# Optimization experiments

Hardware: AMD Instinct MI355X
Metric: run time of the kernel (lower is better)

## Reference

```python
import jax, jax.numpy as jnp
import numpy as np

GRID_SIZE = 25
DAMPING = 0.01


def setup_inputs() -> dict:
    key = jax.random.key(0)
    k1, k2 = jax.random.split(key)
    local_x = jax.random.normal(k1, (1, 4, 1000, 1000), dtype=jnp.float32)
    ms_history = jax.random.normal(k2, (1, 16, 4, 1000, 1000), dtype=jnp.float32)
    return {"local_x": local_x, "ms_history": ms_history}


def _project(local_x, ms_history):
    new_hist = ms_history[0]                      # (nt, nb, nx, ny)
    nt, nb, nx, ny = new_hist.shape
    nb2 = local_x.shape[1]
    ngs = GRID_SIZE
    ngx, ngy = nx // ngs, ny // ngs
    K, P = nb * nt, ngs * ngs
    # tile-ize: (ngx, ngy, K, P) and (ngx, ngy, nb2, P)
    V = new_hist.reshape(K, ngx, ngs, ngy, ngs).transpose(1, 3, 0, 2, 4).reshape(ngx, ngy, K, P)
    X = local_x.reshape(nb2, ngx, ngs, ngy, ngs).transpose(1, 3, 0, 2, 4).reshape(ngx, ngy, nb2, P)
    # batched damped Gram matrix: (ngx, ngy, K, K)
    G = jnp.einsum('xykp,xylp->xykl', V, V) + DAMPING * jnp.eye(K, dtype=V.dtype)
    Ginv = jnp.linalg.inv(G)                      # batched small inverse
    A = jnp.einsum('xycp,xykp->xyck', X, V)       # X @ V^T : (ngx, ngy, nb2, K)
    AG = jnp.einsum('xyck,xykl->xycl', A, Ginv)   # X @ V^T @ inv(G)
    Y = jnp.einsum('xycl,xylp->xycp', AG, V)      # projected tiles: (ngx, ngy, nb2, P)
    # re-assemble spatial image: (1, nb2, nx, ny)
    W = Y.reshape(ngx, ngy, nb2, ngs, ngs).transpose(2, 0, 3, 1, 4).reshape(1, nb2, nx, ny)
    return W


def reference(local_x, ms_history):
    return _project(local_x, ms_history)
```

## Files before the change

kernel.cpp:

```cpp
#include <hip/hip_runtime.h>

#define NGS 25
#define NGX 40
#define NGY 40
#define KK  64
#define NB2 4
#define NYY 1000
#define PTOT 625
#define PC  64
#define NCH 10
#define DAMP 0.01f

typedef __attribute__((ext_vector_type(8))) short short8;
typedef __attribute__((ext_vector_type(4))) float f32x4;

__device__ __forceinline__ short bf16_rn(float x) {
  unsigned u = __float_as_uint(x);
  u = u + 0x7fffu + ((u >> 16) & 1u);
  return (short)(u >> 16);
}
__device__ __forceinline__ float bf16_tof(short s) {
  return __uint_as_float(((unsigned)(unsigned short)s) << 16);
}

__global__ __launch_bounds__(256, 8) void k_gram_solve(
    const float* __restrict__ xin, const float* __restrict__ hist,
    float* __restrict__ AG)
{
  __shared__ __align__(16) short smem[2 * 80 * PC + 2 * 72 * 2];
  short* Vhi = smem;
  short* Vlo = smem + 80 * PC;
  float (*Gs)[KK + 5] = (float (*)[KK + 5])smem;
  float* prow = ((float*)smem) + (2 * 80 * PC) / 2;

  const int tile = blockIdx.x;
  const int gx = tile / NGY, gy = tile % NGY;
  const size_t base = (size_t)(gx * NGS) * NYY + (size_t)(gy * NGS);
  const int tid  = threadIdx.x;
  const int wave = tid >> 6;
  const int lane = tid & 63;
  const int u    = lane >> 4;
  const int col  = lane & 15;

  const int pp = tid & 63;
  const int rb = tid >> 6;

  for (int i = tid + 68 * PC; i < 80 * PC; i += 256) { Vhi[i] = 0; Vlo[i] = 0; }

  f32x4 accG[4];
  #pragma unroll
  for (int j = 0; j < 4; ++j) { accG[j].x = 0.f; accG[j].y = 0.f; accG[j].z = 0.f; accG[j].w = 0.f; }
  f32x4 accX; accX.x = 0.f; accX.y = 0.f; accX.z = 0.f; accX.w = 0.f;

  const int rA = 16 * wave + col;
  const int rX = KK + col;

  #define STW(r, val) { \
    const short h = (short)(__float_as_uint(val) >> 16); \
    const short l = bf16_rn((val) - bf16_tof(h)); \
    const int off = (r) * PC + ((((pp >> 3) ^ ((r) & 7)) << 3) | (pp & 7)); \
    Vhi[off] = h; Vlo[off] = l; }

  for (int ch = 0; ch < NCH; ++ch) {
    const int p = ch * PC + pp;
    const bool inb = (p < PTOT);
    const int px = p / NGS, py = p - px * NGS;
    const size_t a = base + (size_t)px * NYY + py;

    float v0[9], v1[8];
    #pragma unroll
    for (int it = 0; it < 9; ++it)
      v0[it] = inb ? hist[(size_t)(rb + 4 * it) * 1000000 + a] : 0.f;
    #pragma unroll
    for (int it = 0; it < 8; ++it) {
      v1[it] = inb ? ((it < 7) ? hist[(size_t)(rb + 4 * (it + 9)) * 1000000 + a]
                               : xin[(size_t)rb * 1000000 + a]) : 0.f;
    }
    #pragma unroll
    for (int it = 0; it < 9; ++it) STW(rb + 4 * it, v0[it]);
    #pragma unroll
    for (int it = 0; it < 8; ++it) {
      const int r = (it < 7) ? (rb + 4 * (it + 9)) : (KK + rb);
      STW(r, v1[it]);
    }
    __syncthreads();

    #pragma unroll
    for (int t = 0; t < 2; ++t) {
      const int k8 = t * 4 + u;
      #define FRG(P, r) (*(const short8*)&P[(r) * PC + (((k8) ^ ((r) & 7)) << 3)])
      const short8 a_hi = FRG(Vhi, rA);
      const short8 a_lo = FRG(Vlo, rA);
      const short8 x_hi = FRG(Vhi, rX);
      const short8 x_lo = FRG(Vlo, rX);
      short8 b_hi[4], b_lo[4];
      #pragma unroll
      for (int s = 0; s < 4; ++s) {
        b_hi[s] = FRG(Vhi, 16 * s + col);
        b_lo[s] = FRG(Vlo, 16 * s + col);
      }
      #undef FRG
      #pragma unroll
      for (int j = 0; j < 4; ++j) {
        accG[j] = __builtin_amdgcn_mfma_f32_16x16x32_bf16(a_hi, b_hi[j], accG[j], 0, 0, 0);
        accG[j] = __builtin_amdgcn_mfma_f32_16x16x32_bf16(a_hi, b_lo[j], accG[j], 0, 0, 0);
        accG[j] = __builtin_amdgcn_mfma_f32_16x16x32_bf16(a_lo, b_hi[j], accG[j], 0, 0, 0);
      }
      accX = __builtin_amdgcn_mfma_f32_16x16x32_bf16(x_hi, a_hi, accX, 0, 0, 0);
      accX = __builtin_amdgcn_mfma_f32_16x16x32_bf16(x_hi, a_lo, accX, 0, 0, 0);
      accX = __builtin_amdgcn_mfma_f32_16x16x32_bf16(x_lo, a_hi, accX, 0, 0, 0);
    }
    __syncthreads();
  }
  #undef STW

  const int row4 = u * 4;
  #pragma unroll
  for (int j = 0; j < 4; ++j)
    #pragma unroll
    for (int q = 0; q < 4; ++q) {
      const int gr = 16 * wave + row4 + q;
      const int gc = 16 * j + col;
      float g = (q == 0) ? accG[j].x : (q == 1) ? accG[j].y : (q == 2) ? accG[j].z : accG[j].w;
      Gs[gr][gc] = g + ((gr == gc) ? DAMP : 0.f);
    }
  if (lane < 16) {
    Gs[16 * wave + lane][KK + 0] = accX.x;
    Gs[16 * wave + lane][KK + 1] = accX.y;
    Gs[16 * wave + lane][KK + 2] = accX.z;
    Gs[16 * wave + lane][KK + 3] = accX.w;
  }
  __syncthreads();

  const int ei = tid >> 2, eq = tid & 3;
  float v[17];
  #pragma unroll
  for (int jj = 0; jj < 17; ++jj) v[jj] = Gs[ei][4 * jj + eq];

  float myDiag = 1.f;
  if (ei == 0) {
    #pragma unroll
    for (int jj = 0; jj < 17; ++jj) prow[4 * jj + eq] = v[jj];
  }
  __syncthreads();

  #pragma unroll
  for (int k = 0; k < KK; ++k) {
    const float* pr = prow + (k & 1) * 72;
    const float piv = pr[k];
    const float num = __shfl(v[k >> 2], (lane & ~3) | (k & 3), 64);
    const float f = (ei == k) ? 0.f : (num / piv);
    if (ei == k) myDiag = piv;
    #pragma unroll
    for (int jj = (k < 3 ? 0 : (k - 2) >> 2); jj < 17; ++jj)
      v[jj] -= f * pr[4 * jj + eq];
    if (k < KK - 1) {
      if (ei == k + 1) {
        float* pw = prow + ((k + 1) & 1) * 72;
        #pragma unroll
        for (int jj = 0; jj < 17; ++jj) pw[4 * jj + eq] = v[jj];
      }
    }
    __syncthreads();
  }

  AG[(size_t)tile * 256 + eq * 64 + ei] = v[16] / myDiag;
}

__global__ __launch_bounds__(256) void k_project(
    const float* __restrict__ hist, const float* __restrict__ AG,
    float* __restrict__ out)
{
  __shared__ float ag[KK][NB2];
  const int tile = blockIdx.x;
  const int gx = tile / NGY, gy = tile % NGY;
  const size_t base = (size_t)(gx * NGS) * NYY + (size_t)(gy * NGS);
  const int tid = threadIdx.x;
  {
    const int c = tid >> 6, k = tid & 63;
    ag[k][c] = AG[(size_t)tile * 256 + tid];
  }
  __syncthreads();

  const int p1 = tid, p2 = tid + 256, p3 = tid + 512;
  const int a1 = (p1 / NGS) * NYY + (p1 % NGS);
  const int a2 = (p2 / NGS) * NYY + (p2 % NGS);
  const bool has3 = (p3 < PTOT);
  const int a3 = has3 ? ((p3 / NGS) * NYY + (p3 % NGS)) : 0;

  float o1[4] = {0,0,0,0}, o2[4] = {0,0,0,0}, o3[4] = {0,0,0,0};
  const float4* ag4 = (const float4*)ag;

  #pragma unroll 4
  for (int k = 0; k < KK; ++k) {
    const size_t ko = (size_t)k * 1000000 + base;
    const float v1 = hist[ko + a1];
    const float v2 = hist[ko + a2];
    const float v3 = has3 ? hist[ko + a3] : 0.f;
    const float4 w = ag4[k];
    o1[0] += w.x * v1; o1[1] += w.y * v1; o1[2] += w.z * v1; o1[3] += w.w * v1;
    o2[0] += w.x * v2; o2[1] += w.y * v2; o2[2] += w.z * v2; o2[3] += w.w * v2;
    o3[0] += w.x * v3; o3[1] += w.y * v3; o3[2] += w.z * v3; o3[3] += w.w * v3;
  }

  out[(size_t)0 * 1000000 + base + a1] = o1[0];
  out[(size_t)1 * 1000000 + base + a1] = o1[1];
  out[(size_t)2 * 1000000 + base + a1] = o1[2];
  out[(size_t)3 * 1000000 + base + a1] = o1[3];
  out[(size_t)0 * 1000000 + base + a2] = o2[0];
  out[(size_t)1 * 1000000 + base + a2] = o2[1];
  out[(size_t)2 * 1000000 + base + a2] = o2[2];
  out[(size_t)3 * 1000000 + base + a2] = o2[3];
  if (has3) {
    out[(size_t)0 * 1000000 + base + a3] = o3[0];
    out[(size_t)1 * 1000000 + base + a3] = o3[1];
    out[(size_t)2 * 1000000 + base + a3] = o3[2];
    out[(size_t)3 * 1000000 + base + a3] = o3[3];
  }
}

extern "C" void kernel_launch(void* const* d_in, const int* in_sizes, int n_in,
                              void* d_out, int out_size, void* d_ws, size_t ws_size,
                              hipStream_t stream) {
  const float* xin  = (const float*)d_in[0];
  const float* hist = (const float*)d_in[1];
  float* out = (float*)d_out;
  float* AG  = (float*)d_ws;

  k_gram_solve<<<NGX * NGY, 256, 0, stream>>>(xin, hist, AG);
  k_project  <<<NGX * NGY, 256, 0, stream>>>(hist, AG, out);
}
```

Before: 223.7 us.

## Double-buffer LDS chunks and prefetch next chunk's global loads during MFMA

The Gram/solve kernel now keeps two LDS buffers for the hi/lo bf16 split tiles. It issues global loads for the next chunk into registers before the barrier, so they overlap with the MFMA work on the current chunk, and one of the two per-iteration barriers is removed. In exchange, LDS use doubles to about 40KB per block and the launch-bounds occupancy hint drops from 8 to 4 blocks, so fewer waves are resident to hide latency.

```diff
diff --git a/kernel.cpp b/kernel.cpp
--- a/kernel.cpp
+++ b/kernel.cpp
@@ -23,15 +23,13 @@
   return __uint_as_float(((unsigned)(unsigned short)s) << 16);
 }
 
-__global__ __launch_bounds__(256, 8) void k_gram_solve(
+__global__ __launch_bounds__(256, 4) void k_gram_solve(
     const float* __restrict__ xin, const float* __restrict__ hist,
     float* __restrict__ AG)
 {
-  __shared__ __align__(16) short smem[2 * 80 * PC + 2 * 72 * 2];
-  short* Vhi = smem;
-  short* Vlo = smem + 80 * PC;
+  __shared__ __align__(16) short smem[4 * 80 * PC + 288];
   float (*Gs)[KK + 5] = (float (*)[KK + 5])smem;
-  float* prow = ((float*)smem) + (2 * 80 * PC) / 2;
+  float* prow = (float*)(smem + 4 * 80 * PC);
 
   const int tile = blockIdx.x;
   const int gx = tile / NGY, gy = tile % NGY;
@@ -45,8 +43,6 @@
   const int pp = tid & 63;
   const int rb = tid >> 6;
 
-  for (int i = tid + 68 * PC; i < 80 * PC; i += 256) { Vhi[i] = 0; Vlo[i] = 0; }
-
   f32x4 accG[4];
   #pragma unroll
   for (int j = 0; j < 4; ++j) { accG[j].x = 0.f; accG[j].y = 0.f; accG[j].z = 0.f; accG[j].w = 0.f; }
@@ -55,49 +51,54 @@
   const int rA = 16 * wave + col;
   const int rX = KK + col;
 
-  #define STW(r, val) { \
-    const short h = (short)(__float_as_uint(val) >> 16); \
-    const short l = bf16_rn((val) - bf16_tof(h)); \
-    const int off = (r) * PC + ((((pp >> 3) ^ ((r) & 7)) << 3) | (pp & 7)); \
-    Vhi[off] = h; Vlo[off] = l; }
+  float v[17];
+  #define LOADCH(CH) { \
+    const int p = (CH) * PC + pp; \
+    const bool inb = (p < PTOT); \
+    const int px = p / NGS, py = p - px * NGS; \
+    const size_t a = base + (size_t)px * NYY + py; \
+    _Pragma("unroll") \
+    for (int it = 0; it < 17; ++it) { \
+      const int r = rb + 4 * it; \
+      v[it] = inb ? ((it < 16) ? hist[(size_t)r * 1000000 + a] \
+                               : xin[(size_t)rb * 1000000 + a]) : 0.f; \
+    } }
+
+  LOADCH(0);
+  for (int b = 0; b < 2; ++b) {
+    short* Bhi = smem + b * (2 * 80 * PC);
+    short* Blo = Bhi + 80 * PC;
+    for (int i = tid + 68 * PC; i < 80 * PC; i += 256) { Bhi[i] = 0; Blo[i] = 0; }
+  }
 
   for (int ch = 0; ch < NCH; ++ch) {
-    const int p = ch * PC + pp;
-    const bool inb = (p < PTOT);
-    const int px = p / NGS, py = p - px * NGS;
-    const size_t a = base + (size_t)px * NYY + py;
-
-    float v0[9], v1[8];
-    #pragma unroll
-    for (int it = 0; it < 9; ++it)
-      v0[it] = inb ? hist[(size_t)(rb + 4 * it) * 1000000 + a] : 0.f;
-    #pragma unroll
-    for (int it = 0; it < 8; ++it) {
-      v1[it] = inb ? ((it < 7) ? hist[(size_t)(rb + 4 * (it + 9)) * 1000000 + a]
-                               : xin[(size_t)rb * 1000000 + a]) : 0.f;
-    }
-    #pragma unroll
-    for (int it = 0; it < 9; ++it) STW(rb + 4 * it, v0[it]);
-    #pragma unroll
-    for (int it = 0; it < 8; ++it) {
-      const int r = (it < 7) ? (rb + 4 * (it + 9)) : (KK + rb);
-      STW(r, v1[it]);
-    }
+    short* Bhi = smem + (ch & 1) * (2 * 80 * PC);
+    short* Blo = Bhi + 80 * PC;
+
+    #pragma unroll
+    for (int it = 0; it < 17; ++it) {
+      const int r = (it < 16) ? (rb + 4 * it) : (KK + rb);
+      const short h = (short)(__float_as_uint(v[it]) >> 16);
+      const short l = bf16_rn(v[it] - bf16_tof(h));
+      const int off = r * PC + ((((pp >> 3) ^ (r & 7)) << 3) | (pp & 7));
+      Bhi[off] = h; Blo[off] = l;
+    }
+    if (ch < NCH - 1) { LOADCH(ch + 1); }
     __syncthreads();
 
     #pragma unroll
     for (int t = 0; t < 2; ++t) {
       const int k8 = t * 4 + u;
       #define FRG(P, r) (*(const short8*)&P[(r) * PC + (((k8) ^ ((r) & 7)) << 3)])
-      const short8 a_hi = FRG(Vhi, rA);
-      const short8 a_lo = FRG(Vlo, rA);
-      const short8 x_hi = FRG(Vhi, rX);
-      const short8 x_lo = FRG(Vlo, rX);
+      const short8 a_hi = FRG(Bhi, rA);
+      const short8 a_lo = FRG(Blo, rA);
+      const short8 x_hi = FRG(Bhi, rX);
+      const short8 x_lo = FRG(Blo, rX);
       short8 b_hi[4], b_lo[4];
       #pragma unroll
       for (int s = 0; s < 4; ++s) {
-        b_hi[s] = FRG(Vhi, 16 * s + col);
-        b_lo[s] = FRG(Vlo, 16 * s + col);
+        b_hi[s] = FRG(Bhi, 16 * s + col);
+        b_lo[s] = FRG(Blo, 16 * s + col);
       }
       #undef FRG
       #pragma unroll
@@ -110,9 +111,9 @@
       accX = __builtin_amdgcn_mfma_f32_16x16x32_bf16(x_hi, a_lo, accX, 0, 0, 0);
       accX = __builtin_amdgcn_mfma_f32_16x16x32_bf16(x_lo, a_hi, accX, 0, 0, 0);
     }
-    __syncthreads();
-  }
-  #undef STW
+  }
+  #undef LOADCH
+  __syncthreads();
 
   const int row4 = u * 4;
   #pragma unroll
@@ -133,14 +134,14 @@
   __syncthreads();
 
   const int ei = tid >> 2, eq = tid & 3;
-  float v[17];
-  #pragma unroll
-  for (int jj = 0; jj < 17; ++jj) v[jj] = Gs[ei][4 * jj + eq];
+  float w[17];
+  #pragma unroll
+  for (int jj = 0; jj < 17; ++jj) w[jj] = Gs[ei][4 * jj + eq];
 
   float myDiag = 1.f;
   if (ei == 0) {
     #pragma unroll
-    for (int jj = 0; jj < 17; ++jj) prow[4 * jj + eq] = v[jj];
+    for (int jj = 0; jj < 17; ++jj) prow[4 * jj + eq] = w[jj];
   }
   __syncthreads();
 
@@ -148,23 +149,23 @@
   for (int k = 0; k < KK; ++k) {
     const float* pr = prow + (k & 1) * 72;
     const float piv = pr[k];
-    const float num = __shfl(v[k >> 2], (lane & ~3) | (k & 3), 64);
+    const float num = __shfl(w[k >> 2], (lane & ~3) | (k & 3), 64);
     const float f = (ei == k) ? 0.f : (num / piv);
     if (ei == k) myDiag = piv;
     #pragma unroll
     for (int jj = (k < 3 ? 0 : (k - 2) >> 2); jj < 17; ++jj)
-      v[jj] -= f * pr[4 * jj + eq];
+      w[jj] -= f * pr[4 * jj + eq];
     if (k < KK - 1) {
       if (ei == k + 1) {
         float* pw = prow + ((k + 1) & 1) * 72;
         #pragma unroll
-        for (int jj = 0; jj < 17; ++jj) pw[4 * jj + eq] = v[jj];
+        for (int jj = 0; jj < 17; ++jj) pw[4 * jj + eq] = w[jj];
       }
     }
     __syncthreads();
   }
 
-  AG[(size_t)tile * 256 + eq * 64 + ei] = v[16] / myDiag;
+  AG[(size_t)tile * 256 + eq * 64 + ei] = w[16] / myDiag;
 }
 
 __global__ __launch_bounds__(256) void k_project(
```

Result: no change. 224.3 us (+0.3%).
